# Performance work log

Measured on AMD Instinct MI355X. Metric: run time of the kernel, lower is better.

## Reference

```python
import jax, jax.numpy as jnp
import numpy as np
from jax import lax

SMOOTH = 1e-06
SKEL_ITERS = 10  # thresh_width in the original soft_skeletonize


def _maxpool3(x):
    # 3x3 max pool, stride 1, padding 1 on NCHW
    return lax.reduce_window(
        x, -jnp.inf, lax.max,
        window_dimensions=(1, 1, 3, 3),
        window_strides=(1, 1, 1, 1),
        padding=((0, 0), (0, 0), (1, 1), (1, 1)))


def soft_skeletonize(x):
    def body(i, x):
        min_pool_x = -_maxpool3(-x)                      # 3x3 min-pool (erosion)
        contour = jax.nn.relu(_maxpool3(min_pool_x) - min_pool_x)
        return jax.nn.relu(x - contour)
    return lax.fori_loop(0, SKEL_ITERS, body, x)


def norm_intersection(center_line, vessel):
    B, C = center_line.shape[:2]
    clf = center_line.reshape(B, C, -1)
    vf = vessel.reshape(B, C, -1)
    intersection = jnp.sum(clf * vf, axis=-1)
    return (intersection + SMOOTH) / (jnp.sum(clf, axis=-1) + SMOOTH)


def setup_inputs() -> dict:
    key = jax.random.key(0)
    k1, k2 = jax.random.split(key)
    B, C, H, W = 32, 1, 512, 512
    pred = jax.random.uniform(k1, (B, C, H, W), dtype=jnp.float32)
    target = (jax.random.uniform(k2, (B, C, H, W), dtype=jnp.float32) > 0.85).astype(jnp.float32)
    return {"pred": pred, "target": target}


def reference(pred, target):
    cl_pred = soft_skeletonize(pred)
    target_skeleton = soft_skeletonize(target)
    iflat = norm_intersection(cl_pred, target)
    tflat = norm_intersection(target_skeleton, pred)
    intersection = jnp.sum(iflat * tflat)
    return 1.0 - 2.0 * intersection / jnp.sum(iflat + tflat)
```

## Files before the change

kernel.cpp:

```cpp
#include <hip/hip_runtime.h>
#include <math.h>

#define HH 512
#define WW 512
#define BB 32
#define CHUNK 32

__device__ __forceinline__ float min3f(float a, float b, float c) {
    return fminf(fminf(a, b), c);
}
__device__ __forceinline__ float max3f(float a, float b, float c) {
    return fmaxf(fmaxf(a, b), c);
}

__device__ __forceinline__ void loadrowC(const float* __restrict__ img, int R,
                                         int cm4, int c0, int cp4,
                                         bool isL, bool isR, float* xr) {
    const int Rc = R < 0 ? 0 : (R > HH - 1 ? HH - 1 : R);
    const float* rb = img + (size_t)Rc * WW;
    float4 v0 = *(const float4*)(rb + cm4);
    float4 v1 = *(const float4*)(rb + c0);
    float4 v2 = *(const float4*)(rb + cp4);
    xr[0] = v0.x; xr[1] = v0.y; xr[2] = v0.z; xr[3] = v0.w;
    xr[4] = v1.x; xr[5] = v1.y; xr[6] = v1.z; xr[7] = v1.w;
    xr[8] = v2.x; xr[9] = v2.y; xr[10] = v2.z; xr[11] = v2.w;
    if (isL) xr[3] = xr[0];
    if (isR) xr[8] = xr[7];
}

template <int FUSED>
__global__ __launch_bounds__(256) void skel2r_t(const float* __restrict__ srcA,
                                                const float* __restrict__ srcB,
                                                const float* __restrict__ cmpA,
                                                const float* __restrict__ cmpB,
                                                float* __restrict__ dst,
                                                float* __restrict__ partials) {
    const int s = blockIdx.x * 64 + threadIdx.x;
    const int y0 = (blockIdx.y * 4 + threadIdx.y) * CHUNK;
    const int z = blockIdx.z;
    const float* img = (z < BB) ? (srcA + (size_t)z * (HH * WW))
                                : (srcB + (size_t)(z - BB) * (HH * WW));
    const float* cmp = nullptr;
    if (FUSED) cmp = (z < BB) ? (cmpA + (size_t)z * (HH * WW))
                              : (cmpB + (size_t)(z - BB) * (HH * WW));
    float* outp = FUSED ? nullptr : (dst + (size_t)z * (HH * WW));
    const int gx0 = 4 * s;
    const bool isL = (s == 0), isR = (s == 127);
    const int cm4 = isL ? 0 : gx0 - 4;
    const int cp4 = isR ? gx0 : gx0 + 4;

    float hm0a[10], hm0b[10], mn0p[8];
    float hx0a[8], hx0b[8];
    float x0a[8], x0b[8];
    float hm1a[6], hm1b[6], mn1p[4];
    float hx1a[4], hx1b[4];
    float x1a[4], x1b[4];

    #pragma unroll
    for (int i = 0; i < 10; ++i) { hm0a[i] = INFINITY; hm0b[i] = INFINITY; }
    #pragma unroll
    for (int j = 0; j < 8; ++j)  { mn0p[j] = -INFINITY; hx0a[j] = -INFINITY; hx0b[j] = -INFINITY; x0a[j] = INFINITY; x0b[j] = INFINITY; }
    #pragma unroll
    for (int k = 0; k < 6; ++k)  { hm1a[k] = INFINITY; hm1b[k] = INFINITY; }
    #pragma unroll
    for (int m = 0; m < 4; ++m)  { mn1p[m] = -INFINITY; hx1a[m] = -INFINITY; hx1b[m] = -INFINITY; x1a[m] = INFINITY; x1b[m] = INFINITY; }

    float acc0 = 0.0f, acc1 = 0.0f;

    float xA[12], xB[12], xC[12];
    loadrowC(img, y0 - 4, cm4, gx0, cp4, isL, isR, xA);
    loadrowC(img, y0 - 3, cm4, gx0, cp4, isL, isR, xB);
    loadrowC(img, y0 - 2, cm4, gx0, cp4, isL, isR, xC);
    float4 cmpQ0, cmpQ1, cmpQ2;
    cmpQ0.x = cmpQ0.y = cmpQ0.z = cmpQ0.w = 0.f;
    cmpQ1 = cmpQ0; cmpQ2 = cmpQ0;

    #pragma unroll
    for (int rr = 0; rr < CHUNK + 8; ++rr) {
        const int R = y0 - 4 + rr;

        float xD[12];
        if (rr < CHUNK + 5) {
            loadrowC(img, R + 3, cm4, gx0, cp4, isL, isR, xD);
        } else {
            #pragma unroll
            for (int i = 0; i < 12; ++i) xD[i] = INFINITY;
        }

        float4 cmpCur;
        if (FUSED) {
            cmpCur = cmpQ0;
            cmpQ0 = cmpQ1; cmpQ1 = cmpQ2;
            if (rr >= 5 && rr < CHUNK + 5) {
                cmpQ2 = *(const float4*)(cmp + (size_t)(R - 1) * WW + gx0);
            }
        }

        float hm0c[10];
        #pragma unroll
        for (int i = 0; i < 10; ++i) hm0c[i] = min3f(xA[i], xA[i + 1], xA[i + 2]);

        float mn0n[10];
        #pragma unroll
        for (int i = 0; i < 10; ++i) mn0n[i] = min3f(hm0a[i], hm0b[i], hm0c[i]);
        if (!((unsigned)(R - 1) < HH)) {
            #pragma unroll
            for (int i = 0; i < 10; ++i) mn0n[i] = -INFINITY;
        }
        if (isL) { mn0n[0] = -INFINITY; mn0n[1] = -INFINITY; mn0n[2] = -INFINITY; }
        if (isR) { mn0n[7] = -INFINITY; mn0n[8] = -INFINITY; mn0n[9] = -INFINITY; }

        float hx0n[8];
        #pragma unroll
        for (int j = 0; j < 8; ++j) hx0n[j] = max3f(mn0n[j], mn0n[j + 1], mn0n[j + 2]);

        float x1n[8];
        #pragma unroll
        for (int j = 0; j < 8; ++j) {
            float mp = max3f(hx0a[j], hx0b[j], hx0n[j]);
            float ct = fmaxf(mp - mn0p[j], 0.0f);
            x1n[j] = fmaxf(x0a[j] - ct, 0.0f);
        }
        if (!((unsigned)(R - 2) < HH)) {
            #pragma unroll
            for (int j = 0; j < 8; ++j) x1n[j] = INFINITY;
        }
        if (isL) { x1n[0] = INFINITY; x1n[1] = INFINITY; }
        if (isR) { x1n[6] = INFINITY; x1n[7] = INFINITY; }

        float hm1n[6];
        #pragma unroll
        for (int k = 0; k < 6; ++k) hm1n[k] = min3f(x1n[k], x1n[k + 1], x1n[k + 2]);

        float mn1n[6];
        #pragma unroll
        for (int k = 0; k < 6; ++k) mn1n[k] = min3f(hm1a[k], hm1b[k], hm1n[k]);
        if (!((unsigned)(R - 3) < HH)) {
            #pragma unroll
            for (int k = 0; k < 6; ++k) mn1n[k] = -INFINITY;
        }
        if (isL) mn1n[0] = -INFINITY;
        if (isR) mn1n[5] = -INFINITY;

        float hx1n[4];
        #pragma unroll
        for (int m = 0; m < 4; ++m) hx1n[m] = max3f(mn1n[m], mn1n[m + 1], mn1n[m + 2]);

        if (rr >= 8) {
            float o[4];
            #pragma unroll
            for (int m = 0; m < 4; ++m) {
                float mp = max3f(hx1a[m], hx1b[m], hx1n[m]);
                float ct = fmaxf(mp - mn1p[m], 0.0f);
                o[m] = fmaxf(x1a[m] - ct, 0.0f);
            }
            if (FUSED) {
                acc0 += o[0] * cmpCur.x + o[1] * cmpCur.y + o[2] * cmpCur.z + o[3] * cmpCur.w;
                acc1 += o[0] + o[1] + o[2] + o[3];
            } else {
                float4 ov;
                ov.x = o[0]; ov.y = o[1]; ov.z = o[2]; ov.w = o[3];
                *(float4*)(outp + (size_t)(R - 4) * WW + gx0) = ov;
            }
        }

        #pragma unroll
        for (int i = 0; i < 10; ++i) { hm0a[i] = hm0b[i]; hm0b[i] = hm0c[i]; }
        #pragma unroll
        for (int j = 0; j < 8; ++j)  { mn0p[j] = mn0n[j + 1]; hx0a[j] = hx0b[j]; hx0b[j] = hx0n[j]; x0a[j] = x0b[j]; x0b[j] = xA[j + 2]; }
        #pragma unroll
        for (int k = 0; k < 6; ++k)  { hm1a[k] = hm1b[k]; hm1b[k] = hm1n[k]; }
        #pragma unroll
        for (int m = 0; m < 4; ++m)  { mn1p[m] = mn1n[m + 1]; hx1a[m] = hx1b[m]; hx1b[m] = hx1n[m]; x1a[m] = x1b[m]; x1b[m] = x1n[m + 2]; }
        #pragma unroll
        for (int i = 0; i < 12; ++i) { xA[i] = xB[i]; xB[i] = xC[i]; xC[i] = xD[i]; }
    }

    if (FUSED) {
        for (int off = 32; off; off >>= 1) {
            acc0 += __shfl_down(acc0, off);
            acc1 += __shfl_down(acc1, off);
        }
        __shared__ float red[4][2];
        if (threadIdx.x == 0) { red[threadIdx.y][0] = acc0; red[threadIdx.y][1] = acc1; }
        __syncthreads();
        if (threadIdx.x == 0 && threadIdx.y == 0) {
            const int tile = blockIdx.x * gridDim.y + blockIdx.y;
            float* p = partials + ((size_t)z * 16 + tile) * 2;
            p[0] = red[0][0] + red[1][0] + red[2][0] + red[3][0];
            p[1] = red[0][1] + red[1][1] + red[2][1] + red[3][1];
        }
    }
}

__global__ __launch_bounds__(64) void finalize2(const float* __restrict__ partials,
                                                int ntiles,
                                                float* __restrict__ out) {
    const int b = threadIdx.x;
    float iflat = 0.f, tflat = 0.f;
    if (b < BB) {
        float v0 = 0.f, v1 = 0.f, v2 = 0.f, v3 = 0.f;
        for (int t = 0; t < ntiles; ++t) {
            v0 += partials[((size_t)b * 16 + t) * 2 + 0];
            v1 += partials[((size_t)b * 16 + t) * 2 + 1];
            v2 += partials[((size_t)(b + BB) * 16 + t) * 2 + 0];
            v3 += partials[((size_t)(b + BB) * 16 + t) * 2 + 1];
        }
        iflat = (v0 + 1e-6f) / (v1 + 1e-6f);
        tflat = (v2 + 1e-6f) / (v3 + 1e-6f);
    }
    float prod = iflat * tflat;
    float ssum = iflat + tflat;
    for (int off = 32; off; off >>= 1) {
        prod += __shfl_down(prod, off);
        ssum += __shfl_down(ssum, off);
    }
    if (threadIdx.x == 0) out[0] = 1.0f - 2.0f * prod / ssum;
}

extern "C" void kernel_launch(void* const* d_in, const int* in_sizes, int n_in,
                              void* d_out, int out_size, void* d_ws, size_t ws_size,
                              hipStream_t stream) {
    const float* pred = (const float*)d_in[0];
    const float* target = (const float*)d_in[1];
    float* out = (float*)d_out;
    char* ws = (char*)d_ws;
    const size_t N = (size_t)HH * WW;
    const size_t HALF = (size_t)BB * N;
    const size_t IMG32 = HALF * sizeof(float);

    dim3 block(64, 4);
    const int nby = HH / (CHUNK * 4);
    const int ntiles = 2 * nby;

    if (ws_size >= 4 * IMG32 + (1 << 16)) {
        float* A = (float*)ws;
        float* B = (float*)(ws + 2 * IMG32);
        float* partials = (float*)(ws + 4 * IMG32);
        dim3 grid(2, nby, 2 * BB);
        skel2r_t<0><<<grid, block, 0, stream>>>(pred, target, nullptr, nullptr, A, nullptr);
        skel2r_t<0><<<grid, block, 0, stream>>>(A, A + HALF, nullptr, nullptr, B, nullptr);
        skel2r_t<0><<<grid, block, 0, stream>>>(B, B + HALF, nullptr, nullptr, A, nullptr);
        skel2r_t<0><<<grid, block, 0, stream>>>(A, A + HALF, nullptr, nullptr, B, nullptr);
        skel2r_t<1><<<grid, block, 0, stream>>>(B, B + HALF, target, pred, nullptr, partials);
        finalize2<<<1, 64, 0, stream>>>(partials, ntiles, out);
    } else {
        float* b0 = (float*)ws;
        float* b1 = (float*)(ws + IMG32);
        float* partials = (float*)(ws + 2 * IMG32);
        dim3 grid(2, nby, BB);
        skel2r_t<0><<<grid, block, 0, stream>>>(pred, pred, nullptr, nullptr, b0, nullptr);
        skel2r_t<0><<<grid, block, 0, stream>>>(b0, b0, nullptr, nullptr, b1, nullptr);
        skel2r_t<0><<<grid, block, 0, stream>>>(b1, b1, nullptr, nullptr, b0, nullptr);
        skel2r_t<0><<<grid, block, 0, stream>>>(b0, b0, nullptr, nullptr, b1, nullptr);
        skel2r_t<1><<<grid, block, 0, stream>>>(b1, b1, target, target, nullptr, partials);
        skel2r_t<0><<<grid, block, 0, stream>>>(target, target, nullptr, nullptr, b0, nullptr);
        skel2r_t<0><<<grid, block, 0, stream>>>(b0, b0, nullptr, nullptr, b1, nullptr);
        skel2r_t<0><<<grid, block, 0, stream>>>(b1, b1, nullptr, nullptr, b0, nullptr);
        skel2r_t<0><<<grid, block, 0, stream>>>(b0, b0, nullptr, nullptr, b1, nullptr);
        skel2r_t<1><<<grid, block, 0, stream>>>(b1, b1, pred, pred, nullptr,
                                                partials + (size_t)BB * 16 * 2);
        finalize2<<<1, 64, 0, stream>>>(partials, ntiles, out);
    }
}
```

Baseline: 154.8 us.

## Replace two-iteration fused skeleton kernel with single-iteration kernel, ten passes

The kernel now performs one skeletonization iteration per launch instead of two, with a smaller row chunk and launch_bounds hinting four blocks per CU. That means ten full-image passes instead of five. The aim is to cut register pressure and the redundant halo recomputation of the two-step fused pipeline, and to gain occupancy. The cost is doubled global memory traffic and launch count. The ntiles/partials indexing relies on the grid shape. With CHUNK halved, nby doubles, so the partials layout may change.

```diff
diff --git a/kernel.cpp b/kernel.cpp
--- a/kernel.cpp
+++ b/kernel.cpp
@@ -4,7 +4,7 @@
 #define HH 512
 #define WW 512
 #define BB 32
-#define CHUNK 32
+#define CHUNK 16
 
 __device__ __forceinline__ float min3f(float a, float b, float c) {
     return fminf(fminf(a, b), c);
@@ -29,12 +29,12 @@
 }
 
 template <int FUSED>
-__global__ __launch_bounds__(256) void skel2r_t(const float* __restrict__ srcA,
-                                                const float* __restrict__ srcB,
-                                                const float* __restrict__ cmpA,
-                                                const float* __restrict__ cmpB,
-                                                float* __restrict__ dst,
-                                                float* __restrict__ partials) {
+__global__ __launch_bounds__(256, 4) void skel1r_t(const float* __restrict__ srcA,
+                                                   const float* __restrict__ srcB,
+                                                   const float* __restrict__ cmpA,
+                                                   const float* __restrict__ cmpB,
+                                                   float* __restrict__ dst,
+                                                   float* __restrict__ partials) {
     const int s = blockIdx.x * 64 + threadIdx.x;
     const int y0 = (blockIdx.y * 4 + threadIdx.y) * CHUNK;
     const int z = blockIdx.z;
@@ -49,38 +49,30 @@
     const int cm4 = isL ? 0 : gx0 - 4;
     const int cp4 = isR ? gx0 : gx0 + 4;
 
-    float hm0a[10], hm0b[10], mn0p[8];
-    float hx0a[8], hx0b[8];
-    float x0a[8], x0b[8];
-    float hm1a[6], hm1b[6], mn1p[4];
-    float hx1a[4], hx1b[4];
-    float x1a[4], x1b[4];
-
+    float hma[6], hmb[6];
+    float hxa[4], hxb[4], mnp[4];
+    float x0a[4], x0b[4];
     #pragma unroll
-    for (int i = 0; i < 10; ++i) { hm0a[i] = INFINITY; hm0b[i] = INFINITY; }
+    for (int c = 0; c < 6; ++c) { hma[c] = INFINITY; hmb[c] = INFINITY; }
     #pragma unroll
-    for (int j = 0; j < 8; ++j)  { mn0p[j] = -INFINITY; hx0a[j] = -INFINITY; hx0b[j] = -INFINITY; x0a[j] = INFINITY; x0b[j] = INFINITY; }
-    #pragma unroll
-    for (int k = 0; k < 6; ++k)  { hm1a[k] = INFINITY; hm1b[k] = INFINITY; }
-    #pragma unroll
-    for (int m = 0; m < 4; ++m)  { mn1p[m] = -INFINITY; hx1a[m] = -INFINITY; hx1b[m] = -INFINITY; x1a[m] = INFINITY; x1b[m] = INFINITY; }
+    for (int m = 0; m < 4; ++m) { hxa[m] = -INFINITY; hxb[m] = -INFINITY; mnp[m] = -INFINITY; x0a[m] = INFINITY; x0b[m] = INFINITY; }
 
     float acc0 = 0.0f, acc1 = 0.0f;
 
     float xA[12], xB[12], xC[12];
-    loadrowC(img, y0 - 4, cm4, gx0, cp4, isL, isR, xA);
-    loadrowC(img, y0 - 3, cm4, gx0, cp4, isL, isR, xB);
-    loadrowC(img, y0 - 2, cm4, gx0, cp4, isL, isR, xC);
+    loadrowC(img, y0 - 2, cm4, gx0, cp4, isL, isR, xA);
+    loadrowC(img, y0 - 1, cm4, gx0, cp4, isL, isR, xB);
+    loadrowC(img, y0,     cm4, gx0, cp4, isL, isR, xC);
     float4 cmpQ0, cmpQ1, cmpQ2;
     cmpQ0.x = cmpQ0.y = cmpQ0.z = cmpQ0.w = 0.f;
     cmpQ1 = cmpQ0; cmpQ2 = cmpQ0;
 
     #pragma unroll
-    for (int rr = 0; rr < CHUNK + 8; ++rr) {
-        const int R = y0 - 4 + rr;
+    for (int rr = 0; rr < CHUNK + 4; ++rr) {
+        const int R = y0 - 2 + rr;
 
         float xD[12];
-        if (rr < CHUNK + 5) {
+        if (rr < CHUNK + 1) {
             loadrowC(img, R + 3, cm4, gx0, cp4, isL, isR, xD);
         } else {
             #pragma unroll
@@ -91,68 +83,36 @@
         if (FUSED) {
             cmpCur = cmpQ0;
             cmpQ0 = cmpQ1; cmpQ1 = cmpQ2;
-            if (rr >= 5 && rr < CHUNK + 5) {
-                cmpQ2 = *(const float4*)(cmp + (size_t)(R - 1) * WW + gx0);
+            if (rr >= 1 && rr < CHUNK + 1) {
+                cmpQ2 = *(const float4*)(cmp + (size_t)(y0 - 1 + rr) * WW + gx0);
             }
         }
 
-        float hm0c[10];
-        #pragma unroll
-        for (int i = 0; i < 10; ++i) hm0c[i] = min3f(xA[i], xA[i + 1], xA[i + 2]);
-
-        float mn0n[10];
-        #pragma unroll
-        for (int i = 0; i < 10; ++i) mn0n[i] = min3f(hm0a[i], hm0b[i], hm0c[i]);
+        float hmc[6];
+        #pragma unroll
+        for (int c = 0; c < 6; ++c) hmc[c] = min3f(xA[2 + c], xA[3 + c], xA[4 + c]);
+
+        float mnn[6];
+        #pragma unroll
+        for (int c = 0; c < 6; ++c) mnn[c] = min3f(hma[c], hmb[c], hmc[c]);
         if (!((unsigned)(R - 1) < HH)) {
             #pragma unroll
-            for (int i = 0; i < 10; ++i) mn0n[i] = -INFINITY;
-        }
-        if (isL) { mn0n[0] = -INFINITY; mn0n[1] = -INFINITY; mn0n[2] = -INFINITY; }
-        if (isR) { mn0n[7] = -INFINITY; mn0n[8] = -INFINITY; mn0n[9] = -INFINITY; }
-
-        float hx0n[8];
-        #pragma unroll
-        for (int j = 0; j < 8; ++j) hx0n[j] = max3f(mn0n[j], mn0n[j + 1], mn0n[j + 2]);
-
-        float x1n[8];
-        #pragma unroll
-        for (int j = 0; j < 8; ++j) {
-            float mp = max3f(hx0a[j], hx0b[j], hx0n[j]);
-            float ct = fmaxf(mp - mn0p[j], 0.0f);
-            x1n[j] = fmaxf(x0a[j] - ct, 0.0f);
-        }
-        if (!((unsigned)(R - 2) < HH)) {
-            #pragma unroll
-            for (int j = 0; j < 8; ++j) x1n[j] = INFINITY;
-        }
-        if (isL) { x1n[0] = INFINITY; x1n[1] = INFINITY; }
-        if (isR) { x1n[6] = INFINITY; x1n[7] = INFINITY; }
-
-        float hm1n[6];
-        #pragma unroll
-        for (int k = 0; k < 6; ++k) hm1n[k] = min3f(x1n[k], x1n[k + 1], x1n[k + 2]);
-
-        float mn1n[6];
-        #pragma unroll
-        for (int k = 0; k < 6; ++k) mn1n[k] = min3f(hm1a[k], hm1b[k], hm1n[k]);
-        if (!((unsigned)(R - 3) < HH)) {
-            #pragma unroll
-            for (int k = 0; k < 6; ++k) mn1n[k] = -INFINITY;
-        }
-        if (isL) mn1n[0] = -INFINITY;
-        if (isR) mn1n[5] = -INFINITY;
-
-        float hx1n[4];
-        #pragma unroll
-        for (int m = 0; m < 4; ++m) hx1n[m] = max3f(mn1n[m], mn1n[m + 1], mn1n[m + 2]);
-
-        if (rr >= 8) {
+            for (int c = 0; c < 6; ++c) mnn[c] = -INFINITY;
+        }
+        if (isL) mnn[0] = -INFINITY;
+        if (isR) mnn[5] = -INFINITY;
+
+        float hxn[4];
+        #pragma unroll
+        for (int m = 0; m < 4; ++m) hxn[m] = max3f(mnn[m], mnn[m + 1], mnn[m + 2]);
+
+        if (rr >= 4) {
             float o[4];
             #pragma unroll
             for (int m = 0; m < 4; ++m) {
-                float mp = max3f(hx1a[m], hx1b[m], hx1n[m]);
-                float ct = fmaxf(mp - mn1p[m], 0.0f);
-                o[m] = fmaxf(x1a[m] - ct, 0.0f);
+                float mp = max3f(hxa[m], hxb[m], hxn[m]);
+                float ct = fmaxf(mp - mnp[m], 0.0f);
+                o[m] = fmaxf(x0a[m] - ct, 0.0f);
             }
             if (FUSED) {
                 acc0 += o[0] * cmpCur.x + o[1] * cmpCur.y + o[2] * cmpCur.z + o[3] * cmpCur.w;
@@ -160,18 +120,18 @@
             } else {
                 float4 ov;
                 ov.x = o[0]; ov.y = o[1]; ov.z = o[2]; ov.w = o[3];
-                *(float4*)(outp + (size_t)(R - 4) * WW + gx0) = ov;
+                *(float4*)(outp + (size_t)(R - 2) * WW + gx0) = ov;
             }
         }
 
         #pragma unroll
-        for (int i = 0; i < 10; ++i) { hm0a[i] = hm0b[i]; hm0b[i] = hm0c[i]; }
-        #pragma unroll
-        for (int j = 0; j < 8; ++j)  { mn0p[j] = mn0n[j + 1]; hx0a[j] = hx0b[j]; hx0b[j] = hx0n[j]; x0a[j] = x0b[j]; x0b[j] = xA[j + 2]; }
-        #pragma unroll
-        for (int k = 0; k < 6; ++k)  { hm1a[k] = hm1b[k]; hm1b[k] = hm1n[k]; }
-        #pragma unroll
-        for (int m = 0; m < 4; ++m)  { mn1p[m] = mn1n[m + 1]; hx1a[m] = hx1b[m]; hx1b[m] = hx1n[m]; x1a[m] = x1b[m]; x1b[m] = x1n[m + 2]; }
+        for (int c = 0; c < 6; ++c) { hma[c] = hmb[c]; hmb[c] = hmc[c]; }
+        #pragma unroll
+        for (int m = 0; m < 4; ++m) {
+            mnp[m] = mnn[m + 1];
+            hxa[m] = hxb[m]; hxb[m] = hxn[m];
+            x0a[m] = x0b[m]; x0b[m] = xA[4 + m];
+        }
         #pragma unroll
         for (int i = 0; i < 12; ++i) { xA[i] = xB[i]; xB[i] = xC[i]; xC[i] = xD[i]; }
     }
@@ -238,27 +198,34 @@
         float* B = (float*)(ws + 2 * IMG32);
         float* partials = (float*)(ws + 4 * IMG32);
         dim3 grid(2, nby, 2 * BB);
-        skel2r_t<0><<<grid, block, 0, stream>>>(pred, target, nullptr, nullptr, A, nullptr);
-        skel2r_t<0><<<grid, block, 0, stream>>>(A, A + HALF, nullptr, nullptr, B, nullptr);
-        skel2r_t<0><<<grid, block, 0, stream>>>(B, B + HALF, nullptr, nullptr, A, nullptr);
-        skel2r_t<0><<<grid, block, 0, stream>>>(A, A + HALF, nullptr, nullptr, B, nullptr);
-        skel2r_t<1><<<grid, block, 0, stream>>>(B, B + HALF, target, pred, nullptr, partials);
+        skel1r_t<0><<<grid, block, 0, stream>>>(pred, target, nullptr, nullptr, A, nullptr);
+        skel1r_t<0><<<grid, block, 0, stream>>>(A, A + HALF, nullptr, nullptr, B, nullptr);
+        skel1r_t<0><<<grid, block, 0, stream>>>(B, B + HALF, nullptr, nullptr, A, nullptr);
+        skel1r_t<0><<<grid, block, 0, stream>>>(A, A + HALF, nullptr, nullptr, B, nullptr);
+        skel1r_t<0><<<grid, block, 0, stream>>>(B, B + HALF, nullptr, nullptr, A, nullptr);
+        skel1r_t<0><<<grid, block, 0, stream>>>(A, A + HALF, nullptr, nullptr, B, nullptr);
+        skel1r_t<0><<<grid, block, 0, stream>>>(B, B + HALF, nullptr, nullptr, A, nullptr);
+        skel1r_t<0><<<grid, block, 0, stream>>>(A, A + HALF, nullptr, nullptr, B, nullptr);
+        skel1r_t<0><<<grid, block, 0, stream>>>(B, B + HALF, nullptr, nullptr, A, nullptr);
+        skel1r_t<1><<<grid, block, 0, stream>>>(A, A + HALF, target, pred, nullptr, partials);
         finalize2<<<1, 64, 0, stream>>>(partials, ntiles, out);
     } else {
         float* b0 = (float*)ws;
         float* b1 = (float*)(ws + IMG32);
         float* partials = (float*)(ws + 2 * IMG32);
         dim3 grid(2, nby, BB);
-        skel2r_t<0><<<grid, block, 0, stream>>>(pred, pred, nullptr, nullptr, b0, nullptr);
-        skel2r_t<0><<<grid, block, 0, stream>>>(b0, b0, nullptr, nullptr, b1, nullptr);
-        skel2r_t<0><<<grid, block, 0, stream>>>(b1, b1, nullptr, nullptr, b0, nullptr);
-        skel2r_t<0><<<grid, block, 0, stream>>>(b0, b0, nullptr, nullptr, b1, nullptr);
-        skel2r_t<1><<<grid, block, 0, stream>>>(b1, b1, target, target, nullptr, partials);
-        skel2r_t<0><<<grid, block, 0, stream>>>(target, target, nullptr, nullptr, b0, nullptr);
-        skel2r_t<0><<<grid, block, 0, stream>>>(b0, b0, nullptr, nullptr, b1, nullptr);
-        skel2r_t<0><<<grid, block, 0, stream>>>(b1, b1, nullptr, nullptr, b0, nullptr);
-        skel2r_t<0><<<grid, block, 0, stream>>>(b0, b0, nullptr, nullptr, b1, nullptr);
-        skel2r_t<1><<<grid, block, 0, stream>>>(b1, b1, pred, pred, nullptr,
+        skel1r_t<0><<<grid, block, 0, stream>>>(pred, pred, nullptr, nullptr, b0, nullptr);
+        for (int i = 1; i < 9; ++i) {
+            if (i & 1) skel1r_t<0><<<grid, block, 0, stream>>>(b0, b0, nullptr, nullptr, b1, nullptr);
+            else       skel1r_t<0><<<grid, block, 0, stream>>>(b1, b1, nullptr, nullptr, b0, nullptr);
+        }
+        skel1r_t<1><<<grid, block, 0, stream>>>(b0, b0, target, target, nullptr, partials);
+        skel1r_t<0><<<grid, block, 0, stream>>>(target, target, nullptr, nullptr, b0, nullptr);
+        for (int i = 1; i < 9; ++i) {
+            if (i & 1) skel1r_t<0><<<grid, block, 0, stream>>>(b0, b0, nullptr, nullptr, b1, nullptr);
+            else       skel1r_t<0><<<grid, block, 0, stream>>>(b1, b1, nullptr, nullptr, b0, nullptr);
+        }
+        skel1r_t<1><<<grid, block, 0, stream>>>(b0, b0, pred, pred, nullptr,
                                                 partials + (size_t)BB * 16 * 2);
         finalize2<<<1, 64, 0, stream>>>(partials, ntiles, out);
     }
```

New measurement: 262.3 us. +69.4%, slower.
